# Kernel tuning notes

Hardware: AMD Instinct MI355X
Metric: run time of the kernel (lower is better)

Reference implementation:

```python
import jax, jax.numpy as jnp
import numpy as np

B, T, S, H, C, E, V, OOV = 8, 16, 400, 512, 512, 128, 50000, 50


def setup_inputs() -> dict:
    key = jax.random.key(0)
    ks = jax.random.split(key, 24)
    rn = lambda k, shape, s=0.05: jax.random.normal(k, shape, dtype=jnp.float32) * s
    inp = {
        'input_embeddings': rn(ks[0], (B, T, E), 1.0),
        'context': rn(ks[1], (B, 1, C), 1.0),
        'h0': rn(ks[2], (1, B, H), 1.0),
        'c0': rn(ks[3], (1, B, H), 1.0),
        'encoder_outputs': rn(ks[4], (B, S, C), 1.0),
        'encoder_masks': jnp.ones((B, S), jnp.float32),
        'extra_zeros': jnp.zeros((B, OOV), jnp.float32),
        'extended_source_idx': jax.random.randint(ks[5], (B, S), 0, V + OOV),
        'coverage': jnp.zeros((B, 1, S), jnp.float32),
        # LSTM (single layer), torch gate order i,f,g,o
        'W_ih': rn(ks[6], (4 * H, E)), 'W_hh': rn(ks[7], (4 * H, H)),
        'b_ih': rn(ks[8], (4 * H,)), 'b_hh': rn(ks[9], (4 * H,)),
        # attention (concat + coverage)
        'cov_w': rn(ks[10], (H, 1)),
        'energy_w': rn(ks[11], (H, H + C)), 'energy_b': rn(ks[12], (H,)),
        'v': jax.random.uniform(ks[13], (H,), jnp.float32),
        # projections
        'xctx_w': rn(ks[14], (E, E + C)), 'xctx_b': rn(ks[15], (E,)),
        'attnd_w': rn(ks[16], (H, H + C)), 'attnd_b': rn(ks[17], (H,)),
        'vocab_w': rn(ks[18], (V, H)), 'vocab_b': rn(ks[19], (V,)),
        'pgen_w': rn(ks[20], (1, C + H + E)), 'pgen_b': rn(ks[21], (1,)),
    }
    return inp


def reference(input_embeddings, context, h0, c0, encoder_outputs, encoder_masks,
              extra_zeros, extended_source_idx, coverage,
              W_ih, W_hh, b_ih, b_hh, cov_w, energy_w, energy_b, v,
              xctx_w, xctx_b, attnd_w, attnd_b, vocab_w, vocab_b, pgen_w, pgen_b):
    Bn = input_embeddings.shape[0]
    Sn = encoder_outputs.shape[1]
    bidx = jnp.arange(Bn)[:, None]

    def step(carry, emb_t):
        h, c, ctx, cov = carry  # [B,H],[B,H],[B,C],[B,S]
        x = jnp.concatenate([emb_t, ctx], -1) @ xctx_w.T + xctx_b  # [B,E]
        gates = x @ W_ih.T + b_ih + h @ W_hh.T + b_hh
        i, f, g, o = jnp.split(gates, 4, axis=-1)
        c_new = jax.nn.sigmoid(f) * c + jax.nn.sigmoid(i) * jnp.tanh(g)
        h_new = jax.nn.sigmoid(o) * jnp.tanh(c_new)  # [B,H]
        # concat-style Luong attention with coverage
        cov_proj = cov[..., None] * cov_w[:, 0]  # [B,S,H] (Linear(1,H) no bias)
        cat = jnp.concatenate([
            jnp.broadcast_to(h_new[:, None, :], (Bn, Sn, h_new.shape[-1])),
            encoder_outputs], -1)  # [B,S,H+C]
        energy = jnp.tanh(cat @ energy_w.T + energy_b + cov_proj)
        e = energy @ v  # [B,S]
        probs = jax.nn.softmax(e, -1) * encoder_masks
        probs = probs / (probs.sum(-1, keepdims=True) + 1e-12)
        ctx_new = jnp.einsum('bs,bsc->bc', probs, encoder_outputs)
        cov_new = cov + probs
        vocab_dist = jax.nn.softmax(
            (jnp.concatenate([h_new, ctx_new], -1) @ attnd_w.T + attnd_b) @ vocab_w.T + vocab_b, -1)
        p_gen = jax.nn.sigmoid(jnp.concatenate([ctx_new, h_new, x], -1) @ pgen_w.T + pgen_b)  # [B,1]
        ext = jnp.concatenate([vocab_dist * p_gen, extra_zeros], 1)  # [B,V+OOV]
        final = ext.at[bidx, extended_source_idx].add((1.0 - p_gen) * probs)
        return (h_new, c_new, ctx_new, cov_new), (final, probs, cov_new, p_gen)

    init = (h0[0], c0[0], context[:, 0], coverage[:, 0])
    (h, c, ctx, cov), (finals, attns, covs, pgens) = jax.lax.scan(
        step, init, jnp.swapaxes(input_embeddings, 0, 1))
    final_vocab_dists = jnp.swapaxes(finals, 0, 1)  # [B,T,V+OOV]
    attn_dists = jnp.swapaxes(attns, 0, 1)          # [B,T,S]
    coverages = jnp.swapaxes(covs, 0, 1)            # [B,T,S]
    return (final_vocab_dists, ctx[:, None, :], h[None], c[None], attn_dists, pgens[-1], coverages)
```

## Files before the change

### kernel.cpp

```cpp
#include <hip/hip_runtime.h>
#include <math.h>

#define BB 8
#define TT 16
#define SS 400
#define HH 512
#define EE 128
#define VV 50000
#define VE 50050
#define OOVn 50

#define O1 6406400
#define O2 6410496
#define O3 6414592
#define O4 6418688
#define O5 6469888
#define O6 6469896

#define G_OFF    0
#define EWHB_OFF 1179648
#define ENCG_OFF 1310720
#define WXF_OFF  4600000
#define ENCP_OFF 4600000
#define PM_OFF   5700000

typedef __attribute__((ext_vector_type(4))) float floatx4;
typedef __attribute__((ext_vector_type(8))) short short8;
typedef __attribute__((ext_vector_type(8))) unsigned short ushort8_t;
typedef __attribute__((ext_vector_type(4))) unsigned short ushort4_t;

__device__ __forceinline__ float sigm(float x){ return 1.0f/(1.0f+__expf(-x)); }
__device__ __forceinline__ float ftanh(float x){
  float e = __expf(2.0f*x); return 1.0f - 2.0f/(e + 1.0f);
}
__device__ __forceinline__ unsigned short f2bf(float f){
  union { float f; unsigned int u; } v; v.f = f;
  unsigned int u = v.u;
  return (unsigned short)((u + 0x7FFFu + ((u >> 16) & 1u)) >> 16);
}
__device__ __forceinline__ float bfu(unsigned short u){
  union { unsigned int i; float f; } v; v.i = ((unsigned int)u) << 16; return v.f;
}

__global__ __launch_bounds__(256)
void gemm_bt(const float* __restrict__ A, int lda,
             const float* __restrict__ Bm, int ldb,
             const float* __restrict__ bias,
             float* __restrict__ Cm, int ldc,
             int N, int K, int permute, int obf,
             long bsB, long bsC)
{
  __shared__ unsigned short Ash[128*72];
  __shared__ unsigned short Bsh[64*72];
  int tid = threadIdx.x;
  int mbase = blockIdx.x * 128;
  int nbase = blockIdx.y * 64;
  long z = blockIdx.z;
  const float* Bz = Bm + z*bsB;
  int wave = tid >> 6, lane = tid & 63;
  int wm = (wave & 1) * 64, wn = (wave >> 1) * 32;
  int fl = lane & 15, quad = lane >> 4;

  floatx4 acc[4][2];
  for (int i=0;i<4;i++) for(int j=0;j<2;j++) acc[i][j] = (floatx4)(0.0f);

  for (int kc = 0; kc < K; kc += 64) {
    float4 ra[8], rb[4];
#pragma unroll
    for (int i = 0; i < 8; ++i) {
      int idx = tid + i*256;
      int row = idx >> 4;
      int c4 = (idx & 15) << 2;
      ra[i] = *(const float4*)(A + (size_t)(mbase+row)*lda + kc + c4);
    }
#pragma unroll
    for (int i = 0; i < 4; ++i) {
      int idx = tid + i*256;
      int row = idx >> 4;
      int c4 = (idx & 15) << 2;
      int gn = nbase + row;
      if (gn < N) rb[i] = *(const float4*)(Bz + (size_t)gn*ldb + kc + c4);
      else { rb[i].x = 0.f; rb[i].y = 0.f; rb[i].z = 0.f; rb[i].w = 0.f; }
    }
    __syncthreads();
#pragma unroll
    for (int i = 0; i < 8; ++i) {
      int idx = tid + i*256;
      int o = (idx >> 4)*72 + ((idx & 15) << 2);
      Ash[o+0]=f2bf(ra[i].x); Ash[o+1]=f2bf(ra[i].y); Ash[o+2]=f2bf(ra[i].z); Ash[o+3]=f2bf(ra[i].w);
    }
#pragma unroll
    for (int i = 0; i < 4; ++i) {
      int idx = tid + i*256;
      int o = (idx >> 4)*72 + ((idx & 15) << 2);
      Bsh[o+0]=f2bf(rb[i].x); Bsh[o+1]=f2bf(rb[i].y); Bsh[o+2]=f2bf(rb[i].z); Bsh[o+3]=f2bf(rb[i].w);
    }
    __syncthreads();
#pragma unroll
    for (int ks = 0; ks < 2; ++ks) {
      short8 af[4], bfr[2];
      int ko = ks*32 + quad*8;
#pragma unroll
      for (int i=0;i<4;i++) af[i]  = *(const short8*)&Ash[(wm + i*16 + fl)*72 + ko];
#pragma unroll
      for (int j=0;j<2;j++) bfr[j] = *(const short8*)&Bsh[(wn + j*16 + fl)*72 + ko];
#pragma unroll
      for (int i=0;i<4;i++)
#pragma unroll
        for (int j=0;j<2;j++)
          acc[i][j] = __builtin_amdgcn_mfma_f32_16x16x32_bf16(af[i], bfr[j], acc[i][j], 0,0,0);
    }
    __syncthreads();
  }
  for (int i=0;i<4;i++){
    for (int j=0;j<2;j++){
      int nc = nbase + wn + j*16 + fl;
      if (nc >= N) continue;
      float bv = bias ? bias[nc] : 0.0f;
      for (int r=0;r<4;r++){
        int mg = mbase + wm + i*16 + quad*4 + r;
        int orow = permute ? ((mg & 7)*16 + (mg >> 3)) : mg;
        float v = acc[i][j][r] + bv;
        long ci = (long)orow*ldc + nc + z*bsC;
        if (obf) ((unsigned short*)Cm)[ci] = f2bf(v);
        else     Cm[ci] = v;
      }
    }
  }
}

__global__ __launch_bounds__(256)
void gemm_logits(const unsigned short* __restrict__ Abf,
                 const float* __restrict__ Bm, const float* __restrict__ bias,
                 float* __restrict__ out, float* __restrict__ rowsum)
{
  __shared__ unsigned short Ash[128*72];
  __shared__ unsigned short Bsh[64*72];
  __shared__ float rowpart[128];
  int tid = threadIdx.x;
  int nbase = blockIdx.x * 64;
  int wave = tid >> 6, lane = tid & 63;
  int wm = (wave & 1) * 64, wn = (wave >> 1) * 32;
  int fl = lane & 15, quad = lane >> 4;

  floatx4 acc[4][2];
  for (int i=0;i<4;i++) for(int j=0;j<2;j++) acc[i][j] = (floatx4)(0.0f);
  if (tid < 128) rowpart[tid] = 0.f;

  for (int kc = 0; kc < 512; kc += 64) {
    ushort8_t raa[4];
    float4 rb[4];
#pragma unroll
    for (int i = 0; i < 4; ++i) {
      int idx = tid + i*256;
      int row = idx >> 3;
      int c8 = (idx & 7) << 3;
      raa[i] = *(const ushort8_t*)(Abf + (size_t)row*512 + kc + c8);
    }
#pragma unroll
    for (int i = 0; i < 4; ++i) {
      int idx = tid + i*256;
      int row = idx >> 4;
      int c4 = (idx & 15) << 2;
      int gn = nbase + row;
      if (gn < VV) rb[i] = *(const float4*)(Bm + (size_t)gn*512 + kc + c4);
      else { rb[i].x = 0.f; rb[i].y = 0.f; rb[i].z = 0.f; rb[i].w = 0.f; }
    }
    __syncthreads();
#pragma unroll
    for (int i = 0; i < 4; ++i) {
      int idx = tid + i*256;
      int o = (idx >> 3)*72 + ((idx & 7) << 3);
      *(ushort8_t*)&Ash[o] = raa[i];
    }
#pragma unroll
    for (int i = 0; i < 4; ++i) {
      int idx = tid + i*256;
      int o = (idx >> 4)*72 + ((idx & 15) << 2);
      Bsh[o+0]=f2bf(rb[i].x); Bsh[o+1]=f2bf(rb[i].y); Bsh[o+2]=f2bf(rb[i].z); Bsh[o+3]=f2bf(rb[i].w);
    }
    __syncthreads();
#pragma unroll
    for (int ks = 0; ks < 2; ++ks) {
      short8 af[4], bfr[2];
      int ko = ks*32 + quad*8;
#pragma unroll
      for (int i=0;i<4;i++) af[i]  = *(const short8*)&Ash[(wm + i*16 + fl)*72 + ko];
#pragma unroll
      for (int j=0;j<2;j++) bfr[j] = *(const short8*)&Bsh[(wn + j*16 + fl)*72 + ko];
#pragma unroll
      for (int i=0;i<4;i++)
#pragma unroll
        for (int j=0;j<2;j++)
          acc[i][j] = __builtin_amdgcn_mfma_f32_16x16x32_bf16(af[i], bfr[j], acc[i][j], 0,0,0);
    }
    __syncthreads();
  }
  for (int i=0;i<4;i++){
    for (int r=0;r<4;r++){
      int mg = wm + i*16 + quad*4 + r;
      int orow = (mg & 7)*16 + (mg >> 3);
      float rs = 0.f;
      for (int j=0;j<2;j++){
        int nc = nbase + wn + j*16 + fl;
        if (nc < VV) {
          float e = __expf(acc[i][j][r] + bias[nc]);
          out[(size_t)orow*VE + nc] = e;
          rs += e;
        }
      }
      atomicAdd(&rowpart[mg], rs);
    }
  }
  __syncthreads();
  if (tid < 128) {
    int orow = (tid & 7)*16 + (tid >> 3);
    atomicAdd(&rowsum[orow], rowpart[tid]);
  }
}

__global__ __launch_bounds__(256) void p_wx(const float* __restrict__ wih,
    const float* __restrict__ whh, const float* __restrict__ xcw,
    unsigned short* __restrict__ G, float* __restrict__ wxf)
{
  int blk = blockIdx.x, tid = threadIdx.x;
  if (blk < 640) {
    int rt = blk / 10, ct = blk % 10;
    __shared__ float wl[32*128];
    __shared__ float xl[128*64];
    for (int i = tid; i < 4096; i += 256) {
      int r = i >> 7, k = i & 127;
      wl[i] = wih[(size_t)(rt*32+r)*128 + k];
    }
    for (int i = tid; i < 8192; i += 256) {
      int e = i >> 6, c = i & 63;
      xl[i] = xcw[(size_t)e*640 + ct*64 + c];
    }
    __syncthreads();
    for (int o = tid; o < 2048; o += 256) {
      int r = o >> 6, c = o & 63;
      float acc = 0.f;
      for (int e = 0; e < 128; ++e) acc += wl[r*128+e]*xl[e*64+c];
      G[(size_t)(rt*32+r)*1152 + ct*64 + c] = f2bf(acc);
      int col = ct*64 + c;
      if (col >= 128) wxf[(size_t)(rt*32+r)*512 + col - 128] = acc;
    }
  } else {
    int idx = blk - 640;
    for (int q = 0; q < 2; ++q) {
      int n = idx*2048 + q*1024 + tid*4;
      int r = n >> 9, k = n & 511;
      float4 v = *(const float4*)(whh + n);
      ushort4_t s; s[0]=f2bf(v.x); s[1]=f2bf(v.y); s[2]=f2bf(v.z); s[3]=f2bf(v.w);
      *(ushort4_t*)(G + (size_t)r*1152 + 640 + k) = s;
    }
  }
}

__global__ __launch_bounds__(256) void p_small(const float* __restrict__ wih,
    const float* __restrict__ bih, const float* __restrict__ bhh,
    const float* __restrict__ xb, const float* __restrict__ xcw,
    const float* __restrict__ pw, const float* __restrict__ pb,
    float* __restrict__ gb, float* __restrict__ q, float* __restrict__ qb,
    float* __restrict__ d1, float* __restrict__ d2)
{
  int blk = blockIdx.x, tid = threadIdx.x;
  if (blk < 8) {
    __shared__ float xbl[128];
    if (tid < 128) xbl[tid] = xb[tid];
    __syncthreads();
    int r = blk*256 + tid;
    const float* wr = wih + (size_t)r*128;
    float acc = bih[r] + bhh[r];
    for (int e = 0; e < 128; ++e) acc += wr[e]*xbl[e];
    gb[r] = acc;
  } else if (blk < 11) {
    int o = (blk-8)*256 + tid;
    if (o < 640) {
      float acc = 0.f;
      for (int e = 0; e < 128; ++e) acc += pw[1024+e]*xcw[(size_t)e*640 + o];
      q[o] = acc;
    }
  } else {
    if (tid == 0) {
      float acc = 0.f;
      for (int e = 0; e < 128; ++e) acc += pw[1024+e]*xb[e];
      qb[0] = acc + pb[0];
    }
    if (tid < 128) { d1[tid] = 0.f; d2[tid] = 0.f; }
  }
}

__global__ __launch_bounds__(256) void p_cast(const float* __restrict__ ew,
    unsigned short* __restrict__ ewhb)
{
  int blk = blockIdx.x, tid = threadIdx.x;
  for (int q = 0; q < 2; ++q) {
    size_t n = (size_t)blk*2048 + q*1024 + tid*4;
    int p = (int)(n >> 9), k = (int)(n & 511);
    float4 v = *(const float4*)(ew + (size_t)p*1024 + k);
    ushort4_t s; s[0]=f2bf(v.x); s[1]=f2bf(v.y); s[2]=f2bf(v.z); s[3]=f2bf(v.w);
    *(ushort4_t*)(ewhb + n) = s;
  }
}

__global__ __launch_bounds__(256) void s1g(
    const unsigned short* __restrict__ G, const unsigned short* __restrict__ encG,
    const float* __restrict__ gb,
    const float* __restrict__ emb, const float* __restrict__ context,
    const float* __restrict__ h0, const float* __restrict__ c0,
    const float* __restrict__ coverage,
    const float* __restrict__ PM, const float* __restrict__ d1,
    const float* __restrict__ d2,
    float* __restrict__ A1, float* __restrict__ c_cur,
    float* __restrict__ out, int t)
{
  __shared__ float ueh[8][644];
  __shared__ float uc[8][516];
  __shared__ float part[256];
  __shared__ float gl[64];
  __shared__ float invs[8];
  int tid = threadIdx.x, blk = blockIdx.x;

  if (t >= 1 && tid < 8)
    invs[tid] = 1.0f / (d2[(t-1)*8 + tid] + 1e-12f*d1[(t-1)*8 + tid]);
  __syncthreads();

  for (int i = 0; i < 5; ++i) {
    int slot = i*256 + tid;
    int b = slot / 160, sl = slot - b*160;
    if (sl < 32) {
      *(float4*)&ueh[b][sl*4] = *(const float4*)(emb + (size_t)(b*16+t)*128 + sl*4);
    } else {
      int qq = sl - 32;
      const float* hsrc = t ? (A1 + ((size_t)((t-1)*8+b))*1024) : (h0 + b*512);
      *(float4*)&ueh[b][128 + qq*4] = *(const float4*)(hsrc + qq*4);
    }
  }
  if (t == 0) {
    for (int i = 0; i < 4; ++i) {
      int slot = i*256 + tid;
      int b = slot >> 7, sl = slot & 127;
      *(float4*)&uc[b][sl*4] = *(const float4*)(context + b*512 + sl*4);
    }
  } else {
    const float* pmsrc = PM + (size_t)(t-1)*3200;
    for (int i = 0; i < 4; ++i) {
      int slot = i*256 + tid;
      if (slot < 800) {
        int b = slot / 100, sl = slot - b*100;
        float4 p4 = *(const float4*)(pmsrc + b*400 + sl*4);
        float iv = invs[b];
        p4.x *= iv; p4.y *= iv; p4.z *= iv; p4.w *= iv;
        *(float4*)&uc[b][sl*4] = p4;
      }
    }
  }
  __syncthreads();

  if (t >= 1 && blk < 8) {
    int b = blk;
    const float* covprev = (t == 1) ? (coverage + b*400)
                                    : (out + O6 + ((size_t)(b*16 + t-2))*400);
    size_t o = ((size_t)(b*16 + t-1))*400;
    for (int s = tid; s < 400; s += 256) {
      float pr = uc[b][s];
      out[O4 + o + s] = pr;
      out[O6 + o + s] = covprev[s] + pr;
    }
  }

  int dot = tid >> 2, kq = tid & 3;
  int rr = dot >> 3, b = dot & 7;
  int gate = rr >> 1, jj = rr & 1;
  int r = gate*512 + blk*2 + jj;
  const unsigned short* gr = G + (size_t)r*1152;
  float acc = 0.f;
  {
    const unsigned short* gp = gr + kq*8;
    const float* up = &ueh[b][kq*8];
#pragma unroll
    for (int i = 0; i < 4; ++i) {
      ushort8_t w8 = *(const ushort8_t*)(gp + i*32);
      float4 u0 = *(const float4*)(up + i*32);
      float4 u1 = *(const float4*)(up + i*32 + 4);
      acc += bfu(w8[0])*u0.x + bfu(w8[1])*u0.y + bfu(w8[2])*u0.z + bfu(w8[3])*u0.w
           + bfu(w8[4])*u1.x + bfu(w8[5])*u1.y + bfu(w8[6])*u1.z + bfu(w8[7])*u1.w;
    }
  }
  {
    const unsigned short* gp = gr + 640 + kq*8;
    const float* up = &ueh[b][128 + kq*8];
#pragma unroll 4
    for (int i = 0; i < 16; ++i) {
      ushort8_t w8 = *(const ushort8_t*)(gp + i*32);
      float4 u0 = *(const float4*)(up + i*32);
      float4 u1 = *(const float4*)(up + i*32 + 4);
      acc += bfu(w8[0])*u0.x + bfu(w8[1])*u0.y + bfu(w8[2])*u0.z + bfu(w8[3])*u0.w
           + bfu(w8[4])*u1.x + bfu(w8[5])*u1.y + bfu(w8[6])*u1.z + bfu(w8[7])*u1.w;
    }
  }
  if (t == 0) {
    const unsigned short* gp = gr + 128 + kq*8;
    const float* up = &uc[b][kq*8];
#pragma unroll 4
    for (int i = 0; i < 16; ++i) {
      ushort8_t w8 = *(const ushort8_t*)(gp + i*32);
      float4 u0 = *(const float4*)(up + i*32);
      float4 u1 = *(const float4*)(up + i*32 + 4);
      acc += bfu(w8[0])*u0.x + bfu(w8[1])*u0.y + bfu(w8[2])*u0.z + bfu(w8[3])*u0.w
           + bfu(w8[4])*u1.x + bfu(w8[5])*u1.y + bfu(w8[6])*u1.z + bfu(w8[7])*u1.w;
    }
  } else {
    const unsigned short* gp = encG + ((size_t)(b*2048 + r))*400 + kq*8;
    const float* up = &uc[b][kq*8];
#pragma unroll 4
    for (int i = 0; i < 12; ++i) {
      ushort8_t w8 = *(const ushort8_t*)(gp + i*32);
      float4 u0 = *(const float4*)(up + i*32);
      float4 u1 = *(const float4*)(up + i*32 + 4);
      acc += bfu(w8[0])*u0.x + bfu(w8[1])*u0.y + bfu(w8[2])*u0.z + bfu(w8[3])*u0.w
           + bfu(w8[4])*u1.x + bfu(w8[5])*u1.y + bfu(w8[6])*u1.z + bfu(w8[7])*u1.w;
    }
    if (kq < 2) {
      ushort8_t w8 = *(const ushort8_t*)(gp + 12*32);
      float4 u0 = *(const float4*)(up + 12*32);
      float4 u1 = *(const float4*)(up + 12*32 + 4);
      acc += bfu(w8[0])*u0.x + bfu(w8[1])*u0.y + bfu(w8[2])*u0.z + bfu(w8[3])*u0.w
           + bfu(w8[4])*u1.x + bfu(w8[5])*u1.y + bfu(w8[6])*u1.z + bfu(w8[7])*u1.w;
    }
  }
  part[tid] = acc;
  __syncthreads();
  if (tid < 64) {
    int rr2 = tid >> 3;
    int r2 = (rr2 >> 1)*512 + blk*2 + (rr2 & 1);
    gl[tid] = part[tid*4] + part[tid*4+1] + part[tid*4+2] + part[tid*4+3] + gb[r2];
  }
  __syncthreads();
  if (tid < 16) {
    int jj2 = tid >> 3, b2 = tid & 7;
    float gi = gl[(0*2+jj2)*8 + b2];
    float gf = gl[(1*2+jj2)*8 + b2];
    float gg = gl[(2*2+jj2)*8 + b2];
    float go = gl[(3*2+jj2)*8 + b2];
    int j = blk*2 + jj2;
    float cp = t ? c_cur[b2*512+j] : c0[b2*512+j];
    float cn = sigm(gf)*cp + sigm(gi)*ftanh(gg);
    float hn = sigm(go)*ftanh(cn);
    c_cur[b2*512+j] = cn;
    A1[((size_t)(t*8+b2))*1024 + j] = hn;
  }
}

__global__ __launch_bounds__(256) void s2_hp(
    const unsigned short* __restrict__ ewhb, const float* __restrict__ eb,
    const float* __restrict__ A1, float* __restrict__ hp, int t)
{
  __shared__ float hl[8*516];
  __shared__ float part[256];
  int tid = threadIdx.x, pc = blockIdx.x;
  for (int b = 0; b < 8; ++b)
    for (int k = tid; k < 512; k += 256)
      hl[b*516 + k] = A1[((size_t)(t*8+b))*1024 + k];
  __syncthreads();
  int dot = tid >> 2, kq = tid & 3;
  int rr = dot >> 3, b = dot & 7;
  int p = pc*8 + rr;
  const unsigned short* wp = ewhb + (size_t)p*512 + kq*16;
  const float* hh = hl + b*516 + kq*16;
  float acc = 0.f;
#pragma unroll
  for (int i = 0; i < 8; ++i) {
    ushort8_t wa = *(const ushort8_t*)(wp + i*64);
    ushort8_t wb = *(const ushort8_t*)(wp + i*64 + 8);
    float4 h0v = *(const float4*)(hh + i*64);
    float4 h1v = *(const float4*)(hh + i*64 + 4);
    float4 h2v = *(const float4*)(hh + i*64 + 8);
    float4 h3v = *(const float4*)(hh + i*64 + 12);
    acc += bfu(wa[0])*h0v.x + bfu(wa[1])*h0v.y + bfu(wa[2])*h0v.z + bfu(wa[3])*h0v.w
         + bfu(wa[4])*h1v.x + bfu(wa[5])*h1v.y + bfu(wa[6])*h1v.z + bfu(wa[7])*h1v.w
         + bfu(wb[0])*h2v.x + bfu(wb[1])*h2v.y + bfu(wb[2])*h2v.z + bfu(wb[3])*h2v.w
         + bfu(wb[4])*h3v.x + bfu(wb[5])*h3v.y + bfu(wb[6])*h3v.z + bfu(wb[7])*h3v.w;
  }
  part[tid] = acc;
  __syncthreads();
  if (tid < 64) {
    int rr2 = tid >> 3, b2 = tid & 7;
    int p2 = pc*8 + rr2;
    hp[b2*512 + p2] = eb[p2] + part[tid*4] + part[tid*4+1] + part[tid*4+2] + part[tid*4+3];
  }
}

__global__ __launch_bounds__(256) void s3e(
    const unsigned short* __restrict__ encpb, const float* __restrict__ hp,
    const float* __restrict__ vvec, const float* __restrict__ covw,
    const float* __restrict__ masks, const float* __restrict__ coverage,
    const float* __restrict__ out6v, float* __restrict__ PM,
    float* __restrict__ d1, float* __restrict__ d2, int t)
{
  int tid = threadIdx.x;
  int b = blockIdx.x >> 4, sc = blockIdx.x & 15;
  int w = tid >> 6, lane = tid & 63;
  int h0i = lane*8;
  __shared__ float red1[4], red2[4];
  float hpv[8], vv[8], cw[8];
  {
    const float* hpp = hp + b*512 + h0i;
    float4 a0 = *(const float4*)(hpp), a1 = *(const float4*)(hpp+4);
    hpv[0]=a0.x; hpv[1]=a0.y; hpv[2]=a0.z; hpv[3]=a0.w;
    hpv[4]=a1.x; hpv[5]=a1.y; hpv[6]=a1.z; hpv[7]=a1.w;
    float4 v0 = *(const float4*)(vvec+h0i), v1 = *(const float4*)(vvec+h0i+4);
    vv[0]=v0.x; vv[1]=v0.y; vv[2]=v0.z; vv[3]=v0.w;
    vv[4]=v1.x; vv[5]=v1.y; vv[6]=v1.z; vv[7]=v1.w;
    float4 c0v = *(const float4*)(covw+h0i), c1v = *(const float4*)(covw+h0i+4);
    cw[0]=c0v.x; cw[1]=c0v.y; cw[2]=c0v.z; cw[3]=c0v.w;
    cw[4]=c1v.x; cw[5]=c1v.y; cw[6]=c1v.z; cw[7]=c1v.w;
  }
  const float* covp = t ? (out6v + ((size_t)(b*16 + t-1))*400) : (coverage + b*400);
  float a1s = 0.f, a2s = 0.f;
  for (int sl = w; sl < 25; sl += 4) {
    int s = sc*25 + sl;
    float cv = covp[s];
    const unsigned short* ep = encpb + ((size_t)(b*400+s))*512 + h0i;
    ushort8_t e8 = *(const ushort8_t*)ep;
    float acc = 0.f;
#pragma unroll
    for (int i = 0; i < 8; ++i)
      acc += ftanh(hpv[i] + bfu(e8[i]) + cv*cw[i]) * vv[i];
    for (int off = 32; off > 0; off >>= 1) acc += __shfl_down(acc, off);
    if (lane == 0) {
      float pe = __expf(acc);
      float pmv = pe * masks[b*400 + s];
      PM[(size_t)t*3200 + b*400 + s] = pmv;
      a1s += pe; a2s += pmv;
    }
  }
  if (lane == 0) { red1[w] = a1s; red2[w] = a2s; }
  __syncthreads();
  if (tid == 0) {
    atomicAdd(&d1[t*8+b], red1[0]+red1[1]+red1[2]+red1[3]);
    atomicAdd(&d2[t*8+b], red2[0]+red2[1]+red2[2]+red2[3]);
  }
}

__global__ __launch_bounds__(256) void ctx_all(
    const float* __restrict__ PM, const float* __restrict__ d1,
    const float* __restrict__ d2, const float* __restrict__ enc,
    float* __restrict__ A1, float* __restrict__ out)
{
  int tid = threadIdx.x;
  int b = blockIdx.x >> 2, cc = blockIdx.x & 3;
  __shared__ float prl[16][400];
  __shared__ float redbuf[16][128];
  __shared__ float invs[16];
  if (tid < 16) invs[tid] = 1.0f / (d2[tid*8+b] + 1e-12f*d1[tid*8+b]);
  __syncthreads();
  for (int i = 0; i < 7; ++i) {
    int slot = i*256 + tid;
    if (slot < 1600) {
      int tt = slot / 100, sl = slot - tt*100;
      float4 p4 = *(const float4*)(PM + (size_t)tt*3200 + b*400 + sl*4);
      float iv = invs[tt];
      p4.x *= iv; p4.y *= iv; p4.z *= iv; p4.w *= iv;
      *(float4*)&prl[tt][sl*4] = p4;
    }
  }
  __syncthreads();
  if (cc == 0) {
    size_t o15 = ((size_t)(b*16 + 15))*400;
    size_t o14 = ((size_t)(b*16 + 14))*400;
    for (int s = tid; s < 400; s += 256) {
      float pr = prl[15][s];
      out[O4 + o15 + s] = pr;
      out[O6 + o15 + s] = out[O6 + o14 + s] + pr;
    }
  }
  int c = cc*128 + (tid & 127);
  int sg = tid >> 7;
  float acc[16];
#pragma unroll
  for (int tt = 0; tt < 16; ++tt) acc[tt] = 0.f;
  for (int s = sg*200; s < sg*200 + 200; ++s) {
    float ev = enc[((size_t)(b*400 + s))*512 + c];
#pragma unroll
    for (int tt = 0; tt < 16; ++tt) acc[tt] += prl[tt][s]*ev;
  }
  if (sg == 1) {
#pragma unroll
    for (int tt = 0; tt < 16; ++tt) redbuf[tt][tid & 127] = acc[tt];
  }
  __syncthreads();
  if (sg == 0) {
#pragma unroll
    for (int tt = 0; tt < 16; ++tt)
      A1[((size_t)(tt*8+b))*1024 + 512 + c] = acc[tt] + redbuf[tt][tid & 127];
  }
}

__global__ __launch_bounds__(256) void e_pgen(
    const float* __restrict__ A1, const float* __restrict__ c_cur,
    const float* __restrict__ emb, const float* __restrict__ context,
    const float* __restrict__ pw, const float* __restrict__ q,
    const float* __restrict__ qb, float* __restrict__ pgen,
    float* __restrict__ rowsum, float* __restrict__ out)
{
  int blk = blockIdx.x, tid = threadIdx.x;
  if (blk < 128) {
    int m = blk, t = m >> 3, b = m & 7;
    const float* ctxT = A1 + (size_t)m*1024 + 512;
    const float* hT   = A1 + (size_t)m*1024;
    const float* embp = emb + (size_t)(b*16+t)*128;
    const float* ctxP = t ? (A1 + ((size_t)((t-1)*8+b))*1024 + 512) : (context + b*512);
    float acc = 0.f;
    for (int k = tid; k < 512; k += 256)
      acc += pw[k]*ctxT[k] + pw[512+k]*hT[k] + q[128+k]*ctxP[k];
    if (tid < 128) acc += q[tid]*embp[tid];
    for (int off = 32; off > 0; off >>= 1) acc += __shfl_down(acc, off);
    __shared__ float red[4];
    if (!(tid & 63)) red[tid>>6] = acc;
    __syncthreads();
    if (tid == 0) {
      float pg = sigm(red[0]+red[1]+red[2]+red[3] + qb[0]);
      pgen[m] = pg;
      if (t == 15) out[O5 + b] = pg;
    }
  } else if (blk == 128) {
    for (int i = tid; i < 4096; i += 256) {
      int b = i >> 9, j = i & 511;
      out[O1 + i] = A1[((size_t)(120+b))*1024 + 512 + j];
    }
  } else if (blk == 129) {
    for (int i = tid; i < 4096; i += 256) {
      int b = i >> 9, j = i & 511;
      out[O2 + i] = A1[((size_t)(120+b))*1024 + j];
    }
  } else if (blk == 130) {
    for (int i = tid; i < 4096; i += 256) out[O3 + i] = c_cur[i];
  } else {
    if (tid < 128) rowsum[tid] = 0.f;
  }
}

__global__ __launch_bounds__(256) void k_scale(
    float* __restrict__ out, const float* __restrict__ pgen,
    const float* __restrict__ rowsum, const float* __restrict__ ez)
{
  int orow = blockIdx.x, cy = blockIdx.y, tid = threadIdx.x;
  int b = orow >> 4, t = orow & 15;
  float sc = pgen[t*8+b] / rowsum[orow];
  int c0 = cy*6256;
  int c1 = (cy == 7) ? VE : c0 + 6256;
  float* row = out + (size_t)orow*VE;
  for (int c = c0 + tid*4; c < c1; c += 1024) {
    if (c + 4 <= VV && c + 4 <= c1) {
      float4 v = *(float4*)(row + c);
      v.x *= sc; v.y *= sc; v.z *= sc; v.w *= sc;
      *(float4*)(row + c) = v;
    } else {
      for (int e = 0; e < 4; ++e) {
        int cc2 = c + e;
        if (cc2 < c1) row[cc2] = (cc2 < VV) ? row[cc2]*sc : ez[b*OOVn + cc2 - VV];
      }
    }
  }
}

__global__ __launch_bounds__(256) void k_scatter(
    float* __restrict__ out, const float* __restrict__ pgen,
    const int* __restrict__ extidx)
{
  int m = blockIdx.x, tid = threadIdx.x;
  int b = m & 7, t = m >> 3;
  float* row = out + ((size_t)(b*TT + t))*VE;
  float onem = 1.0f - pgen[m];
  const float* pr = out + O4 + ((size_t)(b*TT+t))*SS;
  for (int s = tid; s < SS; s += 256) {
    int ix = extidx[b*SS + s];
    atomicAdd(&row[ix], onem * pr[s]);
  }
}

extern "C" void kernel_launch(void* const* d_in, const int* in_sizes, int n_in,
                              void* d_out, int out_size, void* d_ws, size_t ws_size,
                              hipStream_t stream)
{
  (void)in_sizes; (void)n_in; (void)out_size; (void)ws_size;
  const float* emb      = (const float*)d_in[0];
  const float* context  = (const float*)d_in[1];
  const float* h0       = (const float*)d_in[2];
  const float* c0       = (const float*)d_in[3];
  const float* enc      = (const float*)d_in[4];
  const float* masks    = (const float*)d_in[5];
  const float* ez       = (const float*)d_in[6];
  const int*   extidx   = (const int*)d_in[7];
  const float* coverage = (const float*)d_in[8];
  const float* wih      = (const float*)d_in[9];
  const float* whh      = (const float*)d_in[10];
  const float* bih      = (const float*)d_in[11];
  const float* bhh      = (const float*)d_in[12];
  const float* covw     = (const float*)d_in[13];
  const float* ew       = (const float*)d_in[14];
  const float* eb       = (const float*)d_in[15];
  const float* vvec     = (const float*)d_in[16];
  const float* xw       = (const float*)d_in[17];
  const float* xb       = (const float*)d_in[18];
  const float* aw       = (const float*)d_in[19];
  const float* ab       = (const float*)d_in[20];
  const float* vw       = (const float*)d_in[21];
  const float* vb       = (const float*)d_in[22];
  const float* pw       = (const float*)d_in[23];
  const float* pb       = (const float*)d_in[24];
  float* out = (float*)d_out;

  float* ws = (float*)d_ws;
  float* A1       = ws;
  float* c_cur    = ws + 131072;
  float* hp       = ws + 135168;
  unsigned short* attnd_bf = (unsigned short*)(ws + 139264);
  float* pgen     = ws + 172032;
  float* gb       = ws + 172160;
  float* q        = ws + 174208;
  float* qb       = ws + 174848;
  float* d1       = ws + 174852;
  float* d2       = ws + 174980;
  float* rowsum   = ws + 175108;

  unsigned short* G     = (unsigned short*)(out + G_OFF);
  unsigned short* ewhb  = (unsigned short*)(out + EWHB_OFF);
  unsigned short* encG  = (unsigned short*)(out + ENCG_OFF);
  float*          wxf   = out + WXF_OFF;
  unsigned short* encpb = (unsigned short*)(out + ENCP_OFF);
  float*          PM    = out + PM_OFF;

  p_wx<<<1152, 256, 0, stream>>>(wih, whh, xw, G, wxf);
  p_small<<<12, 256, 0, stream>>>(wih, bih, bhh, xb, xw, pw, pb, gb, q, qb, d1, d2);
  p_cast<<<128, 256, 0, stream>>>(ew, ewhb);
  gemm_bt<<<dim3(16,7,8), 256, 0, stream>>>(wxf, 512, enc, 512,
      (const float*)nullptr, (float*)encG, 400, 400, 512, 0, 1,
      (long)400*512, (long)2048*400);
  gemm_bt<<<dim3(25,8,1), 256, 0, stream>>>(enc, 512, ew + 512, 1024,
      (const float*)nullptr, (float*)encpb, 512, 512, 512, 0, 1, 0, 0);

  for (int t = 0; t < TT; ++t) {
    s1g<<<256, 256, 0, stream>>>(G, encG, gb, emb, context, h0, c0, coverage,
                                 PM, d1, d2, A1, c_cur, out, t);
    s2_hp<<<64, 256, 0, stream>>>(ewhb, eb, A1, hp, t);
    s3e<<<128, 256, 0, stream>>>(encpb, hp, vvec, covw, masks, coverage,
                                 out + O6, PM, d1, d2, t);
  }

  ctx_all<<<32, 256, 0, stream>>>(PM, d1, d2, enc, A1, out);
  e_pgen<<<132, 256, 0, stream>>>(A1, c_cur, emb, context, pw, q, qb, pgen, rowsum, out);
  gemm_bt<<<dim3(1,8,1), 256, 0, stream>>>(A1, 1024, aw, 1024, ab,
      (float*)attnd_bf, 512, 512, 1024, 0, 1, 0, 0);
  gemm_logits<<<782, 256, 0, stream>>>(attnd_bf, vw, vb, out, rowsum);
  k_scale<<<dim3(128,8), 256, 0, stream>>>(out, pgen, rowsum, ez);
  k_scatter<<<128, 256, 0, stream>>>(out, pgen, extidx);
}
```

Before: 805.1 us.

## Replace LDS-staged GEMMs with direct-load MFMA GEMM and fuse attention steps

Swaps the shared-memory staged GEMM kernels for one templated kernel in which each lane loads its MFMA fragments straight from global memory and converts them to bf16, with no LDS or barriers in the main loop. The per-step hidden-projection kernel (s2_hp) and the energy kernel (s3e) are merged, so each block recomputes its batch row's projection in shared memory. This drops one launch per timestep and the hp buffer round trip. The encoder-gate GEMM now reads the bf16 weights already stored in G instead of a separate float copy, and the energy-weight cast moves into p_wx, removing p_cast. Direct global fragment loads give up cross-wave reuse through LDS, and the fused kernel repeats the 512x512 projection in each of 8 blocks per batch row.

```diff
diff --git a/kernel.cpp b/kernel.cpp
--- a/kernel.cpp
+++ b/kernel.cpp
@@ -20,7 +20,6 @@
 #define G_OFF    0
 #define EWHB_OFF 1179648
 #define ENCG_OFF 1310720
-#define WXF_OFF  4600000
 #define ENCP_OFF 4600000
 #define PM_OFF   5700000
 
@@ -41,187 +40,120 @@
 __device__ __forceinline__ float bfu(unsigned short u){
   union { unsigned int i; float f; } v; v.i = ((unsigned int)u) << 16; return v.f;
 }
-
-__global__ __launch_bounds__(256)
-void gemm_bt(const float* __restrict__ A, int lda,
-             const float* __restrict__ Bm, int ldb,
-             const float* __restrict__ bias,
-             float* __restrict__ Cm, int ldc,
-             int N, int K, int permute, int obf,
-             long bsB, long bsC)
-{
-  __shared__ unsigned short Ash[128*72];
-  __shared__ unsigned short Bsh[64*72];
+__device__ __forceinline__ short8 cvt8(float4 a, float4 b){
+  short8 r;
+  r[0]=(short)f2bf(a.x); r[1]=(short)f2bf(a.y); r[2]=(short)f2bf(a.z); r[3]=(short)f2bf(a.w);
+  r[4]=(short)f2bf(b.x); r[5]=(short)f2bf(b.y); r[6]=(short)f2bf(b.z); r[7]=(short)f2bf(b.w);
+  return r;
+}
+
+template<int ABF, int OBF, int EXPO, int PERM>
+__global__ __launch_bounds__(256) void gemm_direct(
+    const void* __restrict__ Ap, int lda,
+    const float* __restrict__ Bm, int ldb,
+    const float* __restrict__ bias,
+    void* __restrict__ Cp, long ldc,
+    int N, int K, long bsB, long bsC,
+    float* __restrict__ rowsum)
+{
+  __shared__ float rowpart[128];
   int tid = threadIdx.x;
   int mbase = blockIdx.x * 128;
   int nbase = blockIdx.y * 64;
-  long z = blockIdx.z;
-  const float* Bz = Bm + z*bsB;
+  const float* Bz = Bm + (long)blockIdx.z * bsB;
   int wave = tid >> 6, lane = tid & 63;
-  int wm = (wave & 1) * 64, wn = (wave >> 1) * 32;
+  int wm = (wave & 1)*64, wn = (wave >> 1)*32;
   int fl = lane & 15, quad = lane >> 4;
+  int koff = quad * 8;
 
   floatx4 acc[4][2];
+#pragma unroll
   for (int i=0;i<4;i++) for(int j=0;j<2;j++) acc[i][j] = (floatx4)(0.0f);
-
-  for (int kc = 0; kc < K; kc += 64) {
-    float4 ra[8], rb[4];
-#pragma unroll
-    for (int i = 0; i < 8; ++i) {
-      int idx = tid + i*256;
-      int row = idx >> 4;
-      int c4 = (idx & 15) << 2;
-      ra[i] = *(const float4*)(A + (size_t)(mbase+row)*lda + kc + c4);
-    }
-#pragma unroll
-    for (int i = 0; i < 4; ++i) {
-      int idx = tid + i*256;
-      int row = idx >> 4;
-      int c4 = (idx & 15) << 2;
-      int gn = nbase + row;
-      if (gn < N) rb[i] = *(const float4*)(Bz + (size_t)gn*ldb + kc + c4);
-      else { rb[i].x = 0.f; rb[i].y = 0.f; rb[i].z = 0.f; rb[i].w = 0.f; }
-    }
-    __syncthreads();
-#pragma unroll
-    for (int i = 0; i < 8; ++i) {
-      int idx = tid + i*256;
-      int o = (idx >> 4)*72 + ((idx & 15) << 2);
-      Ash[o+0]=f2bf(ra[i].x); Ash[o+1]=f2bf(ra[i].y); Ash[o+2]=f2bf(ra[i].z); Ash[o+3]=f2bf(ra[i].w);
-    }
-#pragma unroll
-    for (int i = 0; i < 4; ++i) {
-      int idx = tid + i*256;
-      int o = (idx >> 4)*72 + ((idx & 15) << 2);
-      Bsh[o+0]=f2bf(rb[i].x); Bsh[o+1]=f2bf(rb[i].y); Bsh[o+2]=f2bf(rb[i].z); Bsh[o+3]=f2bf(rb[i].w);
-    }
-    __syncthreads();
-#pragma unroll
-    for (int ks = 0; ks < 2; ++ks) {
-      short8 af[4], bfr[2];
-      int ko = ks*32 + quad*8;
-#pragma unroll
-      for (int i=0;i<4;i++) af[i]  = *(const short8*)&Ash[(wm + i*16 + fl)*72 + ko];
-#pragma unroll
-      for (int j=0;j<2;j++) bfr[j] = *(const short8*)&Bsh[(wn + j*16 + fl)*72 + ko];
+  if (EXPO && tid < 128) rowpart[tid] = 0.f;
+
+  int arow[4];
+#pragma unroll
+  for (int i=0;i<4;i++) arow[i] = mbase + wm + i*16 + fl;
+  int brow[2]; bool bok[2];
+#pragma unroll
+  for (int j=0;j<2;j++){ int gn = nbase + wn + j*16 + fl; bok[j] = gn < N; brow[j] = bok[j] ? gn : 0; }
+
+#pragma unroll 2
+  for (int kc = 0; kc < K; kc += 32) {
+    short8 af[4], bfr[2];
+    if (ABF) {
+      const unsigned short* Au = (const unsigned short*)Ap;
 #pragma unroll
       for (int i=0;i<4;i++)
-#pragma unroll
-        for (int j=0;j<2;j++)
-          acc[i][j] = __builtin_amdgcn_mfma_f32_16x16x32_bf16(af[i], bfr[j], acc[i][j], 0,0,0);
-    }
-    __syncthreads();
-  }
+        af[i] = *(const short8*)(Au + (size_t)arow[i]*lda + kc + koff);
+    } else {
+      const float* Af = (const float*)Ap;
+#pragma unroll
+      for (int i=0;i<4;i++) {
+        const float* p = Af + (size_t)arow[i]*lda + kc + koff;
+        float4 a0 = *(const float4*)p;
+        float4 a1 = *(const float4*)(p+4);
+        af[i] = cvt8(a0, a1);
+      }
+    }
+#pragma unroll
+    for (int j=0;j<2;j++) {
+      if (bok[j]) {
+        const float* p = Bz + (size_t)brow[j]*ldb + kc + koff;
+        float4 b0 = *(const float4*)p;
+        float4 b1 = *(const float4*)(p+4);
+        bfr[j] = cvt8(b0, b1);
+      } else {
+        bfr[j] = (short8)(short)0;
+      }
+    }
+#pragma unroll
+    for (int i=0;i<4;i++)
+#pragma unroll
+      for (int j=0;j<2;j++)
+        acc[i][j] = __builtin_amdgcn_mfma_f32_16x16x32_bf16(af[i], bfr[j], acc[i][j], 0,0,0);
+  }
+
+  if (EXPO) __syncthreads();
+#pragma unroll
   for (int i=0;i<4;i++){
-    for (int j=0;j<2;j++){
-      int nc = nbase + wn + j*16 + fl;
-      if (nc >= N) continue;
-      float bv = bias ? bias[nc] : 0.0f;
-      for (int r=0;r<4;r++){
-        int mg = mbase + wm + i*16 + quad*4 + r;
-        int orow = permute ? ((mg & 7)*16 + (mg >> 3)) : mg;
-        float v = acc[i][j][r] + bv;
-        long ci = (long)orow*ldc + nc + z*bsC;
-        if (obf) ((unsigned short*)Cm)[ci] = f2bf(v);
-        else     Cm[ci] = v;
-      }
-    }
-  }
-}
-
-__global__ __launch_bounds__(256)
-void gemm_logits(const unsigned short* __restrict__ Abf,
-                 const float* __restrict__ Bm, const float* __restrict__ bias,
-                 float* __restrict__ out, float* __restrict__ rowsum)
-{
-  __shared__ unsigned short Ash[128*72];
-  __shared__ unsigned short Bsh[64*72];
-  __shared__ float rowpart[128];
-  int tid = threadIdx.x;
-  int nbase = blockIdx.x * 64;
-  int wave = tid >> 6, lane = tid & 63;
-  int wm = (wave & 1) * 64, wn = (wave >> 1) * 32;
-  int fl = lane & 15, quad = lane >> 4;
-
-  floatx4 acc[4][2];
-  for (int i=0;i<4;i++) for(int j=0;j<2;j++) acc[i][j] = (floatx4)(0.0f);
-  if (tid < 128) rowpart[tid] = 0.f;
-
-  for (int kc = 0; kc < 512; kc += 64) {
-    ushort8_t raa[4];
-    float4 rb[4];
-#pragma unroll
-    for (int i = 0; i < 4; ++i) {
-      int idx = tid + i*256;
-      int row = idx >> 3;
-      int c8 = (idx & 7) << 3;
-      raa[i] = *(const ushort8_t*)(Abf + (size_t)row*512 + kc + c8);
-    }
-#pragma unroll
-    for (int i = 0; i < 4; ++i) {
-      int idx = tid + i*256;
-      int row = idx >> 4;
-      int c4 = (idx & 15) << 2;
-      int gn = nbase + row;
-      if (gn < VV) rb[i] = *(const float4*)(Bm + (size_t)gn*512 + kc + c4);
-      else { rb[i].x = 0.f; rb[i].y = 0.f; rb[i].z = 0.f; rb[i].w = 0.f; }
-    }
-    __syncthreads();
-#pragma unroll
-    for (int i = 0; i < 4; ++i) {
-      int idx = tid + i*256;
-      int o = (idx >> 3)*72 + ((idx & 7) << 3);
-      *(ushort8_t*)&Ash[o] = raa[i];
-    }
-#pragma unroll
-    for (int i = 0; i < 4; ++i) {
-      int idx = tid + i*256;
-      int o = (idx >> 4)*72 + ((idx & 15) << 2);
-      Bsh[o+0]=f2bf(rb[i].x); Bsh[o+1]=f2bf(rb[i].y); Bsh[o+2]=f2bf(rb[i].z); Bsh[o+3]=f2bf(rb[i].w);
-    }
-    __syncthreads();
-#pragma unroll
-    for (int ks = 0; ks < 2; ++ks) {
-      short8 af[4], bfr[2];
-      int ko = ks*32 + quad*8;
-#pragma unroll
-      for (int i=0;i<4;i++) af[i]  = *(const short8*)&Ash[(wm + i*16 + fl)*72 + ko];
-#pragma unroll
-      for (int j=0;j<2;j++) bfr[j] = *(const short8*)&Bsh[(wn + j*16 + fl)*72 + ko];
-#pragma unroll
-      for (int i=0;i<4;i++)
-#pragma unroll
-        for (int j=0;j<2;j++)
-          acc[i][j] = __builtin_amdgcn_mfma_f32_16x16x32_bf16(af[i], bfr[j], acc[i][j], 0,0,0);
-    }
-    __syncthreads();
-  }
-  for (int i=0;i<4;i++){
+#pragma unroll
     for (int r=0;r<4;r++){
-      int mg = wm + i*16 + quad*4 + r;
-      int orow = (mg & 7)*16 + (mg >> 3);
+      int mg = mbase + wm + i*16 + quad*4 + r;
+      int orow = PERM ? ((mg & 7)*16 + (mg >> 3)) : mg;
       float rs = 0.f;
+#pragma unroll
       for (int j=0;j<2;j++){
         int nc = nbase + wn + j*16 + fl;
-        if (nc < VV) {
-          float e = __expf(acc[i][j][r] + bias[nc]);
-          out[(size_t)orow*VE + nc] = e;
+        if (nc >= N) continue;
+        float v = acc[i][j][r] + (bias ? bias[nc] : 0.f);
+        long ci = (long)orow*ldc + nc + (long)blockIdx.z*bsC;
+        if (EXPO) {
+          float e = __expf(v);
+          ((float*)Cp)[ci] = e;
           rs += e;
+        } else if (OBF) {
+          ((unsigned short*)Cp)[ci] = f2bf(v);
+        } else {
+          ((float*)Cp)[ci] = v;
         }
       }
-      atomicAdd(&rowpart[mg], rs);
-    }
-  }
-  __syncthreads();
-  if (tid < 128) {
-    int orow = (tid & 7)*16 + (tid >> 3);
-    atomicAdd(&rowsum[orow], rowpart[tid]);
+      if (EXPO) atomicAdd(&rowpart[mg & 127], rs);
+    }
+  }
+  if (EXPO) {
+    __syncthreads();
+    if (tid < 128) {
+      int orow = (tid & 7)*16 + (tid >> 3);
+      atomicAdd(&rowsum[orow], rowpart[tid]);
+    }
   }
 }
 
 __global__ __launch_bounds__(256) void p_wx(const float* __restrict__ wih,
     const float* __restrict__ whh, const float* __restrict__ xcw,
-    unsigned short* __restrict__ G, float* __restrict__ wxf)
+    const float* __restrict__ ew,
+    unsigned short* __restrict__ G, unsigned short* __restrict__ ewhb)
 {
   int blk = blockIdx.x, tid = threadIdx.x;
   if (blk < 640) {
@@ -242,10 +174,8 @@
       float acc = 0.f;
       for (int e = 0; e < 128; ++e) acc += wl[r*128+e]*xl[e*64+c];
       G[(size_t)(rt*32+r)*1152 + ct*64 + c] = f2bf(acc);
-      int col = ct*64 + c;
-      if (col >= 128) wxf[(size_t)(rt*32+r)*512 + col - 128] = acc;
-    }
-  } else {
+    }
+  } else if (blk < 1152) {
     int idx = blk - 640;
     for (int q = 0; q < 2; ++q) {
       int n = idx*2048 + q*1024 + tid*4;
@@ -253,6 +183,15 @@
       float4 v = *(const float4*)(whh + n);
       ushort4_t s; s[0]=f2bf(v.x); s[1]=f2bf(v.y); s[2]=f2bf(v.z); s[3]=f2bf(v.w);
       *(ushort4_t*)(G + (size_t)r*1152 + 640 + k) = s;
+    }
+  } else {
+    int idx = blk - 1152;
+    for (int q = 0; q < 2; ++q) {
+      size_t n = (size_t)idx*2048 + q*1024 + tid*4;
+      int p = (int)(n >> 9), k = (int)(n & 511);
+      float4 v = *(const float4*)(ew + (size_t)p*1024 + k);
+      ushort4_t s; s[0]=f2bf(v.x); s[1]=f2bf(v.y); s[2]=f2bf(v.z); s[3]=f2bf(v.w);
+      *(ushort4_t*)(ewhb + n) = s;
     }
   }
 }
@@ -291,19 +230,6 @@
   }
 }
 
-__global__ __launch_bounds__(256) void p_cast(const float* __restrict__ ew,
-    unsigned short* __restrict__ ewhb)
-{
-  int blk = blockIdx.x, tid = threadIdx.x;
-  for (int q = 0; q < 2; ++q) {
-    size_t n = (size_t)blk*2048 + q*1024 + tid*4;
-    int p = (int)(n >> 9), k = (int)(n & 511);
-    float4 v = *(const float4*)(ew + (size_t)p*1024 + k);
-    ushort4_t s; s[0]=f2bf(v.x); s[1]=f2bf(v.y); s[2]=f2bf(v.z); s[3]=f2bf(v.w);
-    *(ushort4_t*)(ewhb + n) = s;
-  }
-}
-
 __global__ __launch_bounds__(256) void s1g(
     const unsigned short* __restrict__ G, const unsigned short* __restrict__ encG,
     const float* __restrict__ gb,
@@ -453,61 +379,42 @@
   }
 }
 
-__global__ __launch_bounds__(256) void s2_hp(
+__global__ __launch_bounds__(256) void s23(
     const unsigned short* __restrict__ ewhb, const float* __restrict__ eb,
-    const float* __restrict__ A1, float* __restrict__ hp, int t)
-{
-  __shared__ float hl[8*516];
-  __shared__ float part[256];
-  int tid = threadIdx.x, pc = blockIdx.x;
-  for (int b = 0; b < 8; ++b)
-    for (int k = tid; k < 512; k += 256)
-      hl[b*516 + k] = A1[((size_t)(t*8+b))*1024 + k];
-  __syncthreads();
-  int dot = tid >> 2, kq = tid & 3;
-  int rr = dot >> 3, b = dot & 7;
-  int p = pc*8 + rr;
-  const unsigned short* wp = ewhb + (size_t)p*512 + kq*16;
-  const float* hh = hl + b*516 + kq*16;
-  float acc = 0.f;
-#pragma unroll
-  for (int i = 0; i < 8; ++i) {
-    ushort8_t wa = *(const ushort8_t*)(wp + i*64);
-    ushort8_t wb = *(const ushort8_t*)(wp + i*64 + 8);
-    float4 h0v = *(const float4*)(hh + i*64);
-    float4 h1v = *(const float4*)(hh + i*64 + 4);
-    float4 h2v = *(const float4*)(hh + i*64 + 8);
-    float4 h3v = *(const float4*)(hh + i*64 + 12);
-    acc += bfu(wa[0])*h0v.x + bfu(wa[1])*h0v.y + bfu(wa[2])*h0v.z + bfu(wa[3])*h0v.w
-         + bfu(wa[4])*h1v.x + bfu(wa[5])*h1v.y + bfu(wa[6])*h1v.z + bfu(wa[7])*h1v.w
-         + bfu(wb[0])*h2v.x + bfu(wb[1])*h2v.y + bfu(wb[2])*h2v.z + bfu(wb[3])*h2v.w
-         + bfu(wb[4])*h3v.x + bfu(wb[5])*h3v.y + bfu(wb[6])*h3v.z + bfu(wb[7])*h3v.w;
-  }
-  part[tid] = acc;
-  __syncthreads();
-  if (tid < 64) {
-    int rr2 = tid >> 3, b2 = tid & 7;
-    int p2 = pc*8 + rr2;
-    hp[b2*512 + p2] = eb[p2] + part[tid*4] + part[tid*4+1] + part[tid*4+2] + part[tid*4+3];
-  }
-}
-
-__global__ __launch_bounds__(256) void s3e(
-    const unsigned short* __restrict__ encpb, const float* __restrict__ hp,
+    const float* __restrict__ A1, const unsigned short* __restrict__ encpb,
     const float* __restrict__ vvec, const float* __restrict__ covw,
     const float* __restrict__ masks, const float* __restrict__ coverage,
     const float* __restrict__ out6v, float* __restrict__ PM,
     float* __restrict__ d1, float* __restrict__ d2, int t)
 {
   int tid = threadIdx.x;
-  int b = blockIdx.x >> 4, sc = blockIdx.x & 15;
+  int b = blockIdx.x >> 3, sc = blockIdx.x & 7;
+  __shared__ float hl[512];
+  __shared__ float hps[512];
+  __shared__ float red1[4], red2[4];
+  for (int k = tid; k < 512; k += 256) hl[k] = A1[((size_t)(t*8+b))*1024 + k];
+  __syncthreads();
+#pragma unroll
+  for (int pi = 0; pi < 2; ++pi) {
+    int p = tid + pi*256;
+    const unsigned short* wp = ewhb + (size_t)p*512;
+    float acc = 0.f;
+#pragma unroll 4
+    for (int k = 0; k < 512; k += 8) {
+      ushort8_t w8 = *(const ushort8_t*)(wp + k);
+      float4 u0 = *(const float4*)(hl + k);
+      float4 u1 = *(const float4*)(hl + k + 4);
+      acc += bfu(w8[0])*u0.x + bfu(w8[1])*u0.y + bfu(w8[2])*u0.z + bfu(w8[3])*u0.w
+           + bfu(w8[4])*u1.x + bfu(w8[5])*u1.y + bfu(w8[6])*u1.z + bfu(w8[7])*u1.w;
+    }
+    hps[p] = eb[p] + acc;
+  }
+  __syncthreads();
   int w = tid >> 6, lane = tid & 63;
   int h0i = lane*8;
-  __shared__ float red1[4], red2[4];
   float hpv[8], vv[8], cw[8];
   {
-    const float* hpp = hp + b*512 + h0i;
-    float4 a0 = *(const float4*)(hpp), a1 = *(const float4*)(hpp+4);
+    float4 a0 = *(const float4*)&hps[h0i], a1 = *(const float4*)&hps[h0i+4];
     hpv[0]=a0.x; hpv[1]=a0.y; hpv[2]=a0.z; hpv[3]=a0.w;
     hpv[4]=a1.x; hpv[5]=a1.y; hpv[6]=a1.z; hpv[7]=a1.w;
     float4 v0 = *(const float4*)(vvec+h0i), v1 = *(const float4*)(vvec+h0i+4);
@@ -519,8 +426,8 @@
   }
   const float* covp = t ? (out6v + ((size_t)(b*16 + t-1))*400) : (coverage + b*400);
   float a1s = 0.f, a2s = 0.f;
-  for (int sl = w; sl < 25; sl += 4) {
-    int s = sc*25 + sl;
+  for (int sl = w; sl < 50; sl += 4) {
+    int s = sc*50 + sl;
     float cv = covp[s];
     const unsigned short* ep = encpb + ((size_t)(b*400+s))*512 + h0i;
     ushort8_t e8 = *(const ushort8_t*)ep;
@@ -716,7 +623,6 @@
   float* ws = (float*)d_ws;
   float* A1       = ws;
   float* c_cur    = ws + 131072;
-  float* hp       = ws + 135168;
   unsigned short* attnd_bf = (unsigned short*)(ws + 139264);
   float* pgen     = ws + 172032;
   float* gb       = ws + 172160;
@@ -729,32 +635,33 @@
   unsigned short* G     = (unsigned short*)(out + G_OFF);
   unsigned short* ewhb  = (unsigned short*)(out + EWHB_OFF);
   unsigned short* encG  = (unsigned short*)(out + ENCG_OFF);
-  float*          wxf   = out + WXF_OFF;
   unsigned short* encpb = (unsigned short*)(out + ENCP_OFF);
   float*          PM    = out + PM_OFF;
 
-  p_wx<<<1152, 256, 0, stream>>>(wih, whh, xw, G, wxf);
+  p_wx<<<1280, 256, 0, stream>>>(wih, whh, xw, ew, G, ewhb);
   p_small<<<12, 256, 0, stream>>>(wih, bih, bhh, xb, xw, pw, pb, gb, q, qb, d1, d2);
-  p_cast<<<128, 256, 0, stream>>>(ew, ewhb);
-  gemm_bt<<<dim3(16,7,8), 256, 0, stream>>>(wxf, 512, enc, 512,
-      (const float*)nullptr, (float*)encG, 400, 400, 512, 0, 1,
-      (long)400*512, (long)2048*400);
-  gemm_bt<<<dim3(25,8,1), 256, 0, stream>>>(enc, 512, ew + 512, 1024,
-      (const float*)nullptr, (float*)encpb, 512, 512, 512, 0, 1, 0, 0);
+  gemm_direct<1,1,0,0><<<dim3(16,7,8), 256, 0, stream>>>(
+      (const void*)(G + 128), 1152, enc, 512, (const float*)nullptr,
+      (void*)encG, 400L, 400, 512, (long)400*512, (long)2048*400, nullptr);
+  gemm_direct<0,1,0,0><<<dim3(25,8,1), 256, 0, stream>>>(
+      (const void*)enc, 512, ew + 512, 1024, (const float*)nullptr,
+      (void*)encpb, 512L, 512, 512, 0L, 0L, nullptr);
 
   for (int t = 0; t < TT; ++t) {
     s1g<<<256, 256, 0, stream>>>(G, encG, gb, emb, context, h0, c0, coverage,
                                  PM, d1, d2, A1, c_cur, out, t);
-    s2_hp<<<64, 256, 0, stream>>>(ewhb, eb, A1, hp, t);
-    s3e<<<128, 256, 0, stream>>>(encpb, hp, vvec, covw, masks, coverage,
-                                 out + O6, PM, d1, d2, t);
+    s23<<<64, 256, 0, stream>>>(ewhb, eb, A1, encpb, vvec, covw, masks,
+                                coverage, out + O6, PM, d1, d2, t);
   }
 
   ctx_all<<<32, 256, 0, stream>>>(PM, d1, d2, enc, A1, out);
   e_pgen<<<132, 256, 0, stream>>>(A1, c_cur, emb, context, pw, q, qb, pgen, rowsum, out);
-  gemm_bt<<<dim3(1,8,1), 256, 0, stream>>>(A1, 1024, aw, 1024, ab,
-      (float*)attnd_bf, 512, 512, 1024, 0, 1, 0, 0);
-  gemm_logits<<<782, 256, 0, stream>>>(attnd_bf, vw, vb, out, rowsum);
+  gemm_direct<0,1,0,0><<<dim3(1,8,1), 256, 0, stream>>>(
+      (const void*)A1, 1024, aw, 1024, ab,
+      (void*)attnd_bf, 512L, 512, 1024, 0L, 0L, nullptr);
+  gemm_direct<1,0,1,1><<<dim3(1,782,1), 256, 0, stream>>>(
+      (const void*)attnd_bf, 512, vw, 512, vb,
+      (void*)out, (long)VE, VV, 512, 0L, 0L, rowsum);
   k_scale<<<dim3(128,8), 256, 0, stream>>>(out, pgen, rowsum, ez);
   k_scatter<<<128, 256, 0, stream>>>(out, pgen, extidx);
 }
```

New measurement: 1.211 ms. 50.5% more time.
